# Optimization experiments

Hardware: AMD Instinct MI355X
Metric: run time of the kernel (lower is better)

## Reference

```python
import jax, jax.numpy as jnp
import numpy as np

ACT_BIT = 8
WEIGHT_BIT = 8
GELU_K = 1.4142
GELU_CONST = 14
C0, C1 = -0.2888, -1.769
C2 = 1.0 / C0  # coeff[2] /= coeff[0]


def round_ste(x):
    return x + jax.lax.stop_gradient(jnp.round(x) - x)


def floor_ste(x):
    return x + jax.lax.stop_gradient(jnp.floor(x) - x)


def sym_scale(bit, smin, smax):
    # symmetric_linear_quantization_params
    n = 2 ** (bit - 1) - 1
    return jnp.clip(jnp.maximum(jnp.abs(smin), jnp.abs(smax)), 1e-8, None) / n


def quant_linear(x, sf_in, weight, bias):
    # per-channel symmetric int8 weight quant, int32 bias, scaled int GEMM
    n = 2 ** (WEIGHT_BIT - 1) - 1
    w_sf = sym_scale(WEIGHT_BIT, weight.min(axis=1), weight.max(axis=1))  # [O]
    w_int = jnp.clip(round_ste(weight / w_sf[:, None]), -n - 1, n)       # [O,H]
    bias_sf = w_sf * sf_in                                               # [O]
    b_int = round_ste(bias / bias_sf)
    x_int = x / sf_in                                                    # [B,S,H]
    out_int = jnp.einsum('bsh,oh->bso', x_int, w_int) + b_int
    return out_int * bias_sf, bias_sf


def int_gelu(x, sf):
    # integer polynomial erf approximation (I-BERT IntGELU)
    x_int = x / sf
    sf_e = sf / GELU_K
    b_int = jnp.floor(C1 / sf_e)
    c_int = jnp.floor(C2 / sf_e ** 2)
    sign = jnp.sign(x_int)
    abs_int = jnp.minimum(jnp.abs(x_int), -b_int)
    y_int = sign * ((abs_int + b_int) ** 2 + c_int)
    sf_sig = sf_e ** 2 * C0
    y_int = floor_ste(y_int / 2.0 ** GELU_CONST)
    sf_sig = sf_sig * 2 ** GELU_CONST
    shift_int = jnp.floor(1.0 / sf_sig)
    x_int = x_int * (y_int + shift_int)
    sf_out = sf * sf_sig / 2
    return x_int * sf_out, sf_out


def quant_act(x, pre_sf):
    # QuantAct: requantize to 8 bits via dyadic (frexp) fixed-point multiply
    n = 2 ** (ACT_BIT - 1) - 1
    sf = sym_scale(ACT_BIT, x.min(), x.max())  # scalar
    z_int = jnp.round(x / pre_sf)
    m, e = jnp.frexp(pre_sf / sf)              # pre_sf is per-channel [O]
    m_int = jnp.round(m * 2.0 ** 31)
    out_int = jnp.clip(jnp.round(z_int * m_int / 2.0 ** (31 - e)), -n - 1, n)
    # FixedPointMul backward is identity w.r.t. x (straight-through)
    q_int = x + jax.lax.stop_gradient(out_int - x)
    return q_int * sf, sf


def setup_inputs() -> dict:
    key = jax.random.key(0)
    k1, k2, k3 = jax.random.split(key, 3)
    B, S, H, I = 8, 2048, 1024, 4096
    sf = jnp.array([0.02], dtype=jnp.float32)
    x = jax.random.normal(k1, (B, S, H), dtype=jnp.float32)
    # pre-quantized 8-bit activations on the incoming grid
    x = jnp.clip(jnp.round(x / sf) * sf, -128 * 0.02, 127 * 0.02)
    weight = jax.random.normal(k2, (I, H), dtype=jnp.float32) * 0.02
    bias = jax.random.normal(k3, (I,), dtype=jnp.float32) * 0.01
    return {"hidden_states": x, "hidden_states_scaling_factor": sf,
            "weight": weight, "bias": bias}


def reference(hidden_states, hidden_states_scaling_factor, weight, bias):
    h, sf = quant_linear(hidden_states, hidden_states_scaling_factor, weight, bias)
    h, sf = int_gelu(h, sf)
    h, sf = quant_act(h, sf)
    return h, sf
```

## Files before the change

### kernel.cpp

```cpp
#include <hip/hip_runtime.h>

#define M_TOK 16384
#define K_DIM 1024
#define N_DIM 4096
#define SLABA ((size_t)M_TOK * 64)
#define SLABB ((size_t)N_DIM * 64)

using i32x4 = __attribute__((ext_vector_type(4))) int;
using f32x4 = __attribute__((ext_vector_type(4))) float;

__device__ __forceinline__ float gelu_q(int acc, float4 pa, float4 pb) {
  float xi = (float)acc + pa.x;
  float sgn = (xi > 0.f) ? 1.f : ((xi < 0.f) ? -1.f : 0.f);
  float ab  = fminf(fabsf(xi), -pa.z);
  float tt  = ab + pa.z;
  float yi  = sgn * (tt * tt + pa.w);
  yi = floorf(yi * (1.0f / 16384.0f));
  return xi * (yi + pb.x);
}

__global__ void k_prep_x(const float* __restrict__ x,
                         const float* __restrict__ sfp,
                         char* __restrict__ x8) {
  float r = 1.0f / sfp[0];
  int i4 = blockIdx.x * 256 + threadIdx.x;
  f32x4 v = __builtin_nontemporal_load((const f32x4*)x + i4);
  int c0 = (int)rintf(v.x * r);
  int c1 = (int)rintf(v.y * r);
  int c2 = (int)rintf(v.z * r);
  int c3 = (int)rintf(v.w * r);
  int packed = (c0 & 0xFF) | ((c1 & 0xFF) << 8) | ((c2 & 0xFF) << 16)
             | ((c3 & 0xFF) << 24);
  int m = i4 >> 8, kq = i4 & 255;
  ((int*)(x8 + (size_t)(kq >> 4) * SLABA + (size_t)m * 64))[kq & 15] = packed;
}

__global__ void k_prep_w(const float* __restrict__ W,
                         const float* __restrict__ bias,
                         const float* __restrict__ sfp,
                         char* __restrict__ w8,
                         float4* __restrict__ cA,
                         float4* __restrict__ cB) {
  const int o = blockIdx.x;
  const int t = threadIdx.x;
  float4 wv = ((const float4*)(W + (size_t)o * K_DIM))[t];
  float vmn = fminf(fminf(wv.x, wv.y), fminf(wv.z, wv.w));
  float vmx = fmaxf(fmaxf(wv.x, wv.y), fmaxf(wv.z, wv.w));
#pragma unroll
  for (int off = 32; off; off >>= 1) {
    vmn = fminf(vmn, __shfl_down(vmn, off, 64));
    vmx = fmaxf(vmx, __shfl_down(vmx, off, 64));
  }
  __shared__ float sm[8];
  __shared__ float s_wsf;
  int lane = t & 63, wv_id = t >> 6;
  if (lane == 0) { sm[wv_id] = vmn; sm[4 + wv_id] = vmx; }
  __syncthreads();
  if (t == 0) {
    float mn = fminf(fminf(sm[0], sm[1]), fminf(sm[2], sm[3]));
    float mx = fmaxf(fmaxf(sm[4], sm[5]), fmaxf(sm[6], sm[7]));
    float wsf = fmaxf(fmaxf(fabsf(mn), fabsf(mx)), 1e-8f) / 127.0f;
    s_wsf = wsf;
    float sfin = sfp[0];
    float bsf  = wsf * sfin;
    float bint = rintf(bias[o] / bsf);
    float sfe  = bsf / 1.4142f;
    float bg   = floorf(-1.769f / sfe);
    const float C2F = (float)(1.0 / -0.2888);
    float cg   = floorf(C2F / (sfe * sfe));
    float sfsig = sfe * sfe * (-0.2888f);
    sfsig = sfsig * 16384.0f;
    float shiftint = floorf(1.0f / sfsig);
    float sfout = bsf * sfsig / 2.0f;
    cA[o] = make_float4(bint, bsf, bg, cg);
    cB[o] = make_float4(shiftint, sfout, 0.0f, 0.0f);
  }
  __syncthreads();
  float wsf = s_wsf;
  int q0 = (int)fminf(fmaxf(rintf(wv.x / wsf), -128.f), 127.f);
  int q1 = (int)fminf(fmaxf(rintf(wv.y / wsf), -128.f), 127.f);
  int q2 = (int)fminf(fmaxf(rintf(wv.z / wsf), -128.f), 127.f);
  int q3 = (int)fminf(fmaxf(rintf(wv.w / wsf), -128.f), 127.f);
  int packed = (q0 & 0xFF) | ((q1 & 0xFF) << 8) | ((q2 & 0xFF) << 16)
             | ((q3 & 0xFF) << 24);
  ((int*)(w8 + (size_t)(t >> 4) * SLABB + (size_t)o * 64))[t & 15] = packed;
}

__global__ __launch_bounds__(256) void k_gemm(
    const char* __restrict__ A, const char* __restrict__ B,
    const float4* __restrict__ cA, const float4* __restrict__ cB,
    float* __restrict__ out, float2* __restrict__ pmm) {
  const int t = threadIdx.x;
  const int lane = t & 63;
  const int w = t >> 6;
  const int wm = w >> 1, wn = w & 1;

  const int lin = blockIdx.y * gridDim.x + blockIdx.x;
  const int xcd = lin & 7;
  const int local = lin >> 3;
  const int bx = xcd * 4 + (local & 3);
  const int by = local >> 2;
  const int m0 = by * 128;
  const int n0 = bx * 128;

  const int fr = lane & 15;
  const int loff = fr * 64 + (lane >> 4) * 16;

  const char* Ap = A + (size_t)(m0 + wm * 64) * 64 + loff;
  const char* Bp = B + (size_t)(n0 + wn * 64) * 64 + loff;

  i32x4 acc[4][4] = {};
  i32x4 ax[4], bxr[4], ay[4], byr[4];
#pragma unroll
  for (int i = 0; i < 4; ++i) {
    ax[i]  = *(const i32x4*)(Ap + i * 1024);
    bxr[i] = *(const i32x4*)(Bp + i * 1024);
  }
#pragma unroll
  for (int it = 0; it < K_DIM / 64; it += 2) {
#pragma unroll
    for (int i = 0; i < 4; ++i) {
      ay[i]  = *(const i32x4*)(Ap + (size_t)(it + 1) * SLABA + i * 1024);
      byr[i] = *(const i32x4*)(Bp + (size_t)(it + 1) * SLABB + i * 1024);
    }
#pragma unroll
    for (int mi = 0; mi < 4; ++mi)
#pragma unroll
      for (int ni = 0; ni < 4; ++ni)
        acc[mi][ni] = __builtin_amdgcn_mfma_i32_16x16x64_i8(
            ax[mi], bxr[ni], acc[mi][ni], 0, 0, 0);
    if (it + 2 < K_DIM / 64) {
#pragma unroll
      for (int i = 0; i < 4; ++i) {
        ax[i]  = *(const i32x4*)(Ap + (size_t)(it + 2) * SLABA + i * 1024);
        bxr[i] = *(const i32x4*)(Bp + (size_t)(it + 2) * SLABB + i * 1024);
      }
    }
#pragma unroll
    for (int mi = 0; mi < 4; ++mi)
#pragma unroll
      for (int ni = 0; ni < 4; ++ni)
        acc[mi][ni] = __builtin_amdgcn_mfma_i32_16x16x64_i8(
            ay[mi], byr[ni], acc[mi][ni], 0, 0, 0);
  }

  const int rowb = m0 + wm * 64 + (lane >> 4) * 4;
  const int colb = n0 + wn * 64 + fr;
  float vmin = 3.4e38f, vmax = -3.4e38f;

#pragma unroll
  for (int ni = 0; ni < 4; ++ni) {
    const int col = colb + ni * 16;
    const float4 pa = cA[col];
    const float4 pb = cB[col];
    float qmn = 3.4e38f, qmx = -3.4e38f;
#pragma unroll
    for (int mi = 0; mi < 4; ++mi) {
#pragma unroll
      for (int r = 0; r < 4; ++r) {
        float q = gelu_q(acc[mi][ni][r], pa, pb);
        qmn = fminf(qmn, q);
        qmx = fmaxf(qmx, q);
        __builtin_nontemporal_store(
            q, &out[(size_t)(rowb + mi * 16 + r) * N_DIM + col]);
      }
    }
    float xa = qmn * pb.y, xb = qmx * pb.y;
    vmin = fminf(vmin, fminf(xa, xb));
    vmax = fmaxf(vmax, fmaxf(xa, xb));
  }

#pragma unroll
  for (int off = 32; off; off >>= 1) {
    vmin = fminf(vmin, __shfl_down(vmin, off, 64));
    vmax = fmaxf(vmax, __shfl_down(vmax, off, 64));
  }
  __shared__ float swmn[4], swmx[4];
  if (lane == 0) { swmn[w] = vmin; swmx[w] = vmax; }
  __syncthreads();
  if (t == 0) {
    float bmn = fminf(fminf(swmn[0], swmn[1]), fminf(swmn[2], swmn[3]));
    float bmx = fmaxf(fmaxf(swmx[0], swmx[1]), fmaxf(swmx[2], swmx[3]));
    pmm[lin] = make_float2(bmn, bmx);
  }
}

__global__ void k_scalar(const float2* __restrict__ pmm,
                         const float4* __restrict__ cB,
                         float* __restrict__ cR,
                         float* __restrict__ sfws,
                         float* __restrict__ out_sf) {
  const int t = threadIdx.x;
  float mn = 3.4e38f, mx = -3.4e38f;
  for (int i = t; i < 4096; i += 256) {
    float2 p = pmm[i];
    mn = fminf(mn, p.x);
    mx = fmaxf(mx, p.y);
  }
#pragma unroll
  for (int off = 32; off; off >>= 1) {
    mn = fminf(mn, __shfl_down(mn, off, 64));
    mx = fmaxf(mx, __shfl_down(mx, off, 64));
  }
  __shared__ float sm[8];
  __shared__ float s_sf;
  int lane = t & 63, wid = t >> 6;
  if (lane == 0) { sm[wid] = mn; sm[4 + wid] = mx; }
  __syncthreads();
  if (t == 0) {
    float m0 = fminf(fminf(sm[0], sm[1]), fminf(sm[2], sm[3]));
    float m1 = fmaxf(fmaxf(sm[4], sm[5]), fmaxf(sm[6], sm[7]));
    float sf = fmaxf(fmaxf(fabsf(m0), fabsf(m1)), 1e-8f) / 127.0f;
    s_sf = sf;
    if (blockIdx.x == 0) { sfws[0] = sf; out_sf[0] = sf; }
  }
  __syncthreads();
  float sf = s_sf;
  int o = blockIdx.x * 256 + t;
  float psf = cB[o].y;
  int e;
  float mm = frexpf(psf / sf, &e);
  float mi = rintf(mm * 2147483648.0f);
  cR[o] = mi * ldexpf(1.0f, e - 31);
}

__global__ __launch_bounds__(256) void k_requant(
    float* __restrict__ out, const float* __restrict__ cR,
    const float* __restrict__ sfws) {
  const float sf = sfws[0];
  const size_t n4 = (size_t)M_TOK * N_DIM / 4;
  for (size_t i4 = (size_t)blockIdx.x * 256 + threadIdx.x; i4 < n4;
       i4 += (size_t)gridDim.x * 256) {
    f32x4 v = __builtin_nontemporal_load((const f32x4*)out + i4);
    int col4 = (int)(i4 & (N_DIM / 4 - 1));
    float4 c = ((const float4*)cR)[col4];
    v.x = fminf(fmaxf(rintf(rintf(v.x) * c.x), -128.f), 127.f) * sf;
    v.y = fminf(fmaxf(rintf(rintf(v.y) * c.y), -128.f), 127.f) * sf;
    v.z = fminf(fmaxf(rintf(rintf(v.z) * c.z), -128.f), 127.f) * sf;
    v.w = fminf(fmaxf(rintf(rintf(v.w) * c.w), -128.f), 127.f) * sf;
    __builtin_nontemporal_store(v, (f32x4*)out + i4);
  }
}

extern "C" void kernel_launch(void* const* d_in, const int* in_sizes, int n_in,
                              void* d_out, int out_size, void* d_ws, size_t ws_size,
                              hipStream_t stream) {
  const float* x    = (const float*)d_in[0];
  const float* sfp  = (const float*)d_in[1];
  const float* W    = (const float*)d_in[2];
  const float* bias = (const float*)d_in[3];
  float* out = (float*)d_out;

  char* ws = (char*)d_ws;
  char* x8 = ws;
  char* w8 = ws + (size_t)M_TOK * K_DIM;
  char* tail = ws + (size_t)M_TOK * K_DIM + (size_t)N_DIM * K_DIM;
  float4* cA = (float4*)tail;
  float4* cB = (float4*)(tail + (size_t)N_DIM * 16);
  float* cR  = (float*)(tail + (size_t)N_DIM * 32);
  float2* pmm = (float2*)(tail + (size_t)N_DIM * 36);
  float* sfws = (float*)(tail + (size_t)N_DIM * 36 + 32768);

  k_prep_x<<<(M_TOK * K_DIM / 4) / 256, 256, 0, stream>>>(x, sfp, x8);
  k_prep_w<<<N_DIM, 256, 0, stream>>>(W, bias, sfp, w8, cA, cB);
  k_gemm<<<dim3(N_DIM / 128, M_TOK / 128), 256, 0, stream>>>(
      x8, w8, cA, cB, out, pmm);
  k_scalar<<<N_DIM / 256, 256, 0, stream>>>(pmm, cB, cR, sfws,
                                            out + (size_t)M_TOK * N_DIM);
  k_requant<<<8192, 256, 0, stream>>>(out, cR, sfws);
}
```

Measured before the change: 542.1 us.

## Stage GEMM tiles through LDS with direct global-to-LDS double buffering

Replaces the per-wave direct register loads of A/B fragments from global memory with cooperative global_load_lds copies into double-buffered shared tiles, then reads fragments from LDS. This means each block tile is fetched once instead of each wave pair reloading the same rows, cutting redundant global/L2 traffic. It adds a __syncthreads per K step and LDS read latency, and drops the previous two-step register prefetch unroll.

```diff
diff --git a/kernel.cpp b/kernel.cpp
--- a/kernel.cpp
+++ b/kernel.cpp
@@ -8,6 +8,12 @@
 
 using i32x4 = __attribute__((ext_vector_type(4))) int;
 using f32x4 = __attribute__((ext_vector_type(4))) float;
+
+__device__ __forceinline__ void gld16(char* lds, const char* g) {
+  __builtin_amdgcn_global_load_lds(
+      (const __attribute__((address_space(1))) void*)g,
+      (__attribute__((address_space(3))) void*)lds, 16, 0, 0);
+}
 
 __device__ __forceinline__ float gelu_q(int acc, float4 pa, float4 pb) {
   float xi = (float)acc + pa.x;
@@ -104,44 +110,58 @@
   const int n0 = bx * 128;
 
   const int fr = lane & 15;
-  const int loff = fr * 64 + (lane >> 4) * 16;
-
-  const char* Ap = A + (size_t)(m0 + wm * 64) * 64 + loff;
-  const char* Bp = B + (size_t)(n0 + wn * 64) * 64 + loff;
+  const int hi16 = (lane >> 4) * 16;
+
+  __shared__ char Ab[2][8192];
+  __shared__ char Bb[2][8192];
+
+  int aoff[4], boff[4];
+#pragma unroll
+  for (int i = 0; i < 4; ++i) {
+    aoff[i] = (wm * 64 + i * 16 + fr) * 64 + hi16;
+    boff[i] = (wn * 64 + i * 16 + fr) * 64 + hi16;
+  }
+
+  const char* Abase = A + (size_t)m0 * 64;
+  const char* Bbase = B + (size_t)n0 * 64;
+  const int c0 = w * 1024 + lane * 16;
+  const int c1 = (w + 4) * 1024 + lane * 16;
+  const int l0 = w * 1024, l1 = (w + 4) * 1024;
+
+  {
+    const char* As = Abase;
+    const char* Bs = Bbase;
+    gld16(&Ab[0][l0], As + c0);
+    gld16(&Ab[0][l1], As + c1);
+    gld16(&Bb[0][l0], Bs + c0);
+    gld16(&Bb[0][l1], Bs + c1);
+  }
+  __syncthreads();
 
   i32x4 acc[4][4] = {};
-  i32x4 ax[4], bxr[4], ay[4], byr[4];
-#pragma unroll
-  for (int i = 0; i < 4; ++i) {
-    ax[i]  = *(const i32x4*)(Ap + i * 1024);
-    bxr[i] = *(const i32x4*)(Bp + i * 1024);
-  }
-#pragma unroll
-  for (int it = 0; it < K_DIM / 64; it += 2) {
+  for (int it = 0; it < K_DIM / 64; ++it) {
+    const int cur = it & 1;
+    if (it + 1 < K_DIM / 64) {
+      const char* As = Abase + (size_t)(it + 1) * SLABA;
+      const char* Bs = Bbase + (size_t)(it + 1) * SLABB;
+      gld16(&Ab[cur ^ 1][l0], As + c0);
+      gld16(&Ab[cur ^ 1][l1], As + c1);
+      gld16(&Bb[cur ^ 1][l0], Bs + c0);
+      gld16(&Bb[cur ^ 1][l1], Bs + c1);
+    }
+    i32x4 af[4], bf[4];
 #pragma unroll
     for (int i = 0; i < 4; ++i) {
-      ay[i]  = *(const i32x4*)(Ap + (size_t)(it + 1) * SLABA + i * 1024);
-      byr[i] = *(const i32x4*)(Bp + (size_t)(it + 1) * SLABB + i * 1024);
+      af[i] = *(const i32x4*)(&Ab[cur][aoff[i]]);
+      bf[i] = *(const i32x4*)(&Bb[cur][boff[i]]);
     }
 #pragma unroll
     for (int mi = 0; mi < 4; ++mi)
 #pragma unroll
       for (int ni = 0; ni < 4; ++ni)
         acc[mi][ni] = __builtin_amdgcn_mfma_i32_16x16x64_i8(
-            ax[mi], bxr[ni], acc[mi][ni], 0, 0, 0);
-    if (it + 2 < K_DIM / 64) {
-#pragma unroll
-      for (int i = 0; i < 4; ++i) {
-        ax[i]  = *(const i32x4*)(Ap + (size_t)(it + 2) * SLABA + i * 1024);
-        bxr[i] = *(const i32x4*)(Bp + (size_t)(it + 2) * SLABB + i * 1024);
-      }
-    }
-#pragma unroll
-    for (int mi = 0; mi < 4; ++mi)
-#pragma unroll
-      for (int ni = 0; ni < 4; ++ni)
-        acc[mi][ni] = __builtin_amdgcn_mfma_i32_16x16x64_i8(
-            ay[mi], byr[ni], acc[mi][ni], 0, 0, 0);
+            af[mi], bf[ni], acc[mi][ni], 0, 0, 0);
+    __syncthreads();
   }
 
   const int rowb = m0 + wm * 64 + (lane >> 4) * 4;
```

Result: faster. 488.3 us (median of 2 runs) (-9.9%).
